# Optimization experiments

Measured on AMD Instinct MI355X. Metric: run time of the kernel, lower is better.

## Reference

```python
import jax, jax.numpy as jnp
import numpy as np

B, G, D, L, NH = 4, 30, 320, 4, 8
DK = D // NH
S = G * G
FF = 4 * D
EPS = 1e-5

FLOAT_KEYS = ['pe', 'in_emb_w', 'in_emb_b', 'wq', 'bq', 'wk', 'bk', 'wv', 'bv', 'wo', 'bo',
              'ln_a_g', 'ln_a_b', 'dist_emb', 'dir_emb', 'w_rot', 'b_rot', 'w_refl', 'b_refl',
              'w_tr', 'b_tr', 'w_sc', 'b_sc', 'tn_w1', 'tn_b1', 'tn_w2', 'tn_b2', 'tn_w3', 'tn_b3',
              'ff_w1', 'ff_b1', 'ff_w2', 'ff_b2', 'ln2_g', 'ln2_b', 'ck1', 'cb1', 'ck3', 'cb3',
              'ck5', 'cb5', 'ck7', 'cb7', 'fus_w', 'fus_b', 'op_w1', 'op_b1', 'op_w2', 'op_b2',
              'op_w3', 'op_b3']


def _make_pe():
    # Faithful vectorization of GeometricPositionalEncoding's triple loop.
    pe = np.zeros((G, G, D), dtype=np.float32)
    i = np.arange(0, D // 2, 2)                       # 0,2,...,158
    div = 10000.0 ** (i / D)
    h = np.arange(G, dtype=np.float64)
    sh = np.sin(h[:, None] / div)[:, None, :]
    ch = np.cos(h[:, None] / div)[:, None, :]
    pe[:, :, i] = sh
    pe[:, :, i + 1] = ch
    sw = np.sin(h[:, None] / div)[None, :, :]
    cw = np.cos(h[:, None] / div)[None, :, :]
    pe[:, :, i + D // 2] = sw
    pe[:, :, i + D // 2 + 1] = cw
    hh, ww = np.meshgrid(np.arange(G), np.arange(G), indexing='ij')
    c = G // 2
    pe[:, :, -4] = np.sqrt((hh - c) ** 2 + (ww - c) ** 2) / G   # overwrites last 4 dims, as in torch
    pe[:, :, -3] = hh / G
    pe[:, :, -2] = ww / G
    pe[:, :, -1] = (hh + ww) / (2 * G)
    return pe


def _make_geo_indices():
    # Precompute _compute_geometric_bias index tables (distance bin, direction octant).
    idx = np.arange(S)
    hc, wc = idx // G, idx % G
    dh = hc[None, :] - hc[:, None]                    # h2 - h1 at [i, j]
    dw = wc[None, :] - wc[:, None]
    dist = np.minimum(np.sqrt(dh ** 2 + dw ** 2).astype(np.int32), 59)
    ang = np.arctan2(dh.astype(np.float64), dw.astype(np.float64))
    dirn = ((ang + np.pi) / (2 * np.pi / 8)).astype(np.int32) % 8
    dirn[(dh == 0) & (dw == 0)] = 0
    return dist.astype(np.int32), dirn.astype(np.int32)


def _ln(x, g, b):
    m = x.mean(-1, keepdims=True)
    v = ((x - m) ** 2).mean(-1, keepdims=True)
    return (x - m) * jax.lax.rsqrt(v + EPS) * g + b


def _gelu(x):
    return jax.nn.gelu(x, approximate=False)  # torch nn.GELU default (erf)


def _forward(p, input_grid, dist_idx, dir_idx):
    x = jax.nn.one_hot(input_grid[:, 0], 10, dtype=jnp.float32)   # [B,G,G,10]
    x = x @ p['in_emb_w'] + p['in_emb_b']                          # [B,G,G,D]
    x = x + p['pe'][None]
    scale = 1.0 / np.sqrt(DK)
    for l in range(L):
        xs = x.reshape(B, S, D)
        def heads(w, b):
            return (xs @ w + b).reshape(B, S, NH, DK).transpose(0, 2, 1, 3)
        q = heads(p['wq'][l], p['bq'][l])
        k = heads(p['wk'][l], p['bk'][l])
        v = heads(p['wv'][l], p['bv'][l])
        # geometric bias via embedding gathers: [S,S,NH] -> [NH,S,S]
        bias = p['dist_emb'][l][dist_idx] + p['dir_emb'][l][dir_idx]
        scores = jnp.einsum('bhsd,bhtd->bhst', q, k) * scale + bias.transpose(2, 0, 1)[None]
        attn = jax.nn.softmax(scores, axis=-1)
        out = jnp.einsum('bhst,bhtd->bhsd', attn, v).transpose(0, 2, 1, 3).reshape(B, S, D)
        xs = _ln(out @ p['wo'][l] + p['bo'][l] + xs, p['ln_a_g'][l], p['ln_a_b'][l])
        # geometric transformation module
        g = xs.mean(1)                                              # [B,D] global mean over H,W
        tp = jnp.concatenate([
            jax.nn.softmax(g @ p['w_rot'][l] + p['b_rot'][l], axis=-1),
            jax.nn.softmax(g @ p['w_refl'][l] + p['b_refl'][l], axis=-1),
            jnp.tanh(g @ p['w_tr'][l] + p['b_tr'][l]),
            jax.nn.softmax(g @ p['w_sc'][l] + p['b_sc'][l], axis=-1)], axis=-1)   # [B,17]
        ti = jnp.concatenate([xs, jnp.broadcast_to(tp[:, None, :], (B, S, 17))], axis=-1)
        t = _gelu(ti @ p['tn_w1'][l] + p['tn_b1'][l])
        t = _gelu(t @ p['tn_w2'][l] + p['tn_b2'][l])
        t = t @ p['tn_w3'][l] + p['tn_b3'][l]
        xs = xs + 0.3 * t
        # feed-forward with post-LN residual
        f = _gelu(xs @ p['ff_w1'][l] + p['ff_b1'][l]) @ p['ff_w2'][l] + p['ff_b2'][l]
        xs = _ln(f + xs, p['ln2_g'][l], p['ln2_b'][l])
        x = xs.reshape(B, G, G, D)
    # multiscale conv fusion (NHWC, SAME padding == torch padding=k//2 for odd k)
    dn = ('NHWC', 'HWIO', 'NHWC')
    feats = [jax.nn.relu(jax.lax.conv_general_dilated(x, p['ck%d' % kk], (1, 1), 'SAME',
                                                      dimension_numbers=dn) + p['cb%d' % kk])
             for kk in (1, 3, 5, 7)]
    fused = jnp.concatenate(feats, axis=-1) @ p['fus_w'] + p['fus_b']
    h1 = _gelu(fused @ p['op_w1'] + p['op_b1'])
    h2 = _gelu(h1 @ p['op_w2'] + p['op_b2'])
    return h2 @ p['op_w3'] + p['op_b3']                            # [B,G,G,10] logits


def setup_inputs():
    key = jax.random.key(0)
    ks = iter(jax.random.split(key, 80))
    w = lambda *s: (0.02 * jax.random.normal(next(ks), s)).astype(jnp.float32)
    z = lambda *s: jnp.zeros(s, jnp.float32)
    inp = dict(
        input_grid=jax.random.randint(next(ks), (B, 1, G, G), 0, 10, dtype=jnp.int32),
        pe=jnp.asarray(_make_pe()),
        in_emb_w=w(10, D), in_emb_b=z(D),
        wq=w(L, D, D), bq=z(L, D), wk=w(L, D, D), bk=z(L, D),
        wv=w(L, D, D), bv=z(L, D), wo=w(L, D, D), bo=z(L, D),
        ln_a_g=jnp.ones((L, D), jnp.float32), ln_a_b=z(L, D),
        dist_emb=w(L, 60, NH), dir_emb=w(L, 8, NH),
        w_rot=w(L, D, 4), b_rot=z(L, 4), w_refl=w(L, D, 8), b_refl=z(L, 8),
        w_tr=w(L, D, 2), b_tr=z(L, 2), w_sc=w(L, D, 3), b_sc=z(L, 3),
        tn_w1=w(L, D + 17, 2 * D), tn_b1=z(L, 2 * D),
        tn_w2=w(L, 2 * D, D), tn_b2=z(L, D),
        tn_w3=w(L, D, D), tn_b3=z(L, D),
        ff_w1=w(L, D, FF), ff_b1=z(L, FF), ff_w2=w(L, FF, D), ff_b2=z(L, D),
        ln2_g=jnp.ones((L, D), jnp.float32), ln2_b=z(L, D),
        ck1=w(1, 1, D, D), cb1=z(D), ck3=w(3, 3, D, D), cb3=z(D),
        ck5=w(5, 5, D, D), cb5=z(D), ck7=w(7, 7, D, D), cb7=z(D),
        fus_w=w(4 * D, D), fus_b=z(D),
        op_w1=w(D, D // 2), op_b1=z(D // 2),
        op_w2=w(D // 2, D // 4), op_b2=z(D // 4),
        op_w3=w(D // 4, 10), op_b3=z(10),
    )
    di, dr = _make_geo_indices()
    inp['dist_idx'] = jnp.asarray(di)
    inp['dir_idx'] = jnp.asarray(dr)
    return inp


def reference(input_grid, dist_idx, dir_idx, pe, in_emb_w, in_emb_b, wq, bq, wk, bk, wv, bv, wo, bo,
              ln_a_g, ln_a_b, dist_emb, dir_emb, w_rot, b_rot, w_refl, b_refl, w_tr, b_tr, w_sc, b_sc,
              tn_w1, tn_b1, tn_w2, tn_b2, tn_w3, tn_b3, ff_w1, ff_b1, ff_w2, ff_b2, ln2_g, ln2_b,
              ck1, cb1, ck3, cb3, ck5, cb5, ck7, cb7, fus_w, fus_b,
              op_w1, op_b1, op_w2, op_b2, op_w3, op_b3):
    p = dict(zip(FLOAT_KEYS, (pe, in_emb_w, in_emb_b, wq, bq, wk, bk, wv, bv, wo, bo,
                              ln_a_g, ln_a_b, dist_emb, dir_emb, w_rot, b_rot, w_refl, b_refl,
                              w_tr, b_tr, w_sc, b_sc, tn_w1, tn_b1, tn_w2, tn_b2, tn_w3, tn_b3,
                              ff_w1, ff_b1, ff_w2, ff_b2, ln2_g, ln2_b, ck1, cb1, ck3, cb3,
                              ck5, cb5, ck7, cb7, fus_w, fus_b, op_w1, op_b1, op_w2, op_b2,
                              op_w3, op_b3)))
    return _forward(p, input_grid, dist_idx, dir_idx)
```

## Files before the change

### kernel.cpp

```cpp
#include <hip/hip_runtime.h>
#include <hip/hip_bf16.h>

#define BB 4
#define GG_ 30
#define DD 320
#define LL 4
#define NHH 8
#define DKK 40
#define SS 900
#define BS 3600
#define FFD 1280
#define LDK 72

typedef __attribute__((ext_vector_type(8))) short short8;
typedef __attribute__((ext_vector_type(4))) short short4v;
typedef __attribute__((ext_vector_type(4))) float f32x4;

__device__ __forceinline__ float gelu_f(float x) {
    return 0.5f * x * (1.0f + erff(x * 0.70710678118654752f));
}

__device__ __forceinline__ float bfbits2f(short b) {
    return __uint_as_float(((unsigned)(unsigned short)b) << 16);
}

__device__ __forceinline__ void convt_tile(const float* __restrict__ s,
                                           __hip_bfloat16* __restrict__ d,
                                           int K, int N, int Kpad, int kb, int nb) {
    __shared__ float t[32][33];
    const int tx = threadIdx.x, ty = threadIdx.y;
#pragma unroll
    for (int i = 0; i < 4; ++i) {
        int k = kb + ty + i * 8, n = nb + tx;
        t[ty + i * 8][tx] = (k < K && n < N) ? s[(size_t)k * N + n] : 0.f;
    }
    __syncthreads();
#pragma unroll
    for (int i = 0; i < 4; ++i) {
        int n = nb + ty + i * 8, k = kb + tx;
        if (n < N && k < Kpad) d[(size_t)n * Kpad + k] = __float2bfloat16(t[tx][ty + i * 8]);
    }
}

__global__ __launch_bounds__(256) void allconvt_kernel(
    const float* wo, const float* tnw1, const float* tnw2, const float* tnw3,
    const float* ffw1, const float* ffw2, const float* ck1, const float* ck3,
    const float* ck5, const float* ck7, const float* fusw, const float* opw1,
    __hip_bfloat16* WOT, __hip_bfloat16* TN1T, __hip_bfloat16* TN2T, __hip_bfloat16* TN3T,
    __hip_bfloat16* FF1T, __hip_bfloat16* FF2T, __hip_bfloat16* CK1T, __hip_bfloat16* CK3T,
    __hip_bfloat16* CK5T, __hip_bfloat16* CK7T, __hip_bfloat16* FUST, __hip_bfloat16* OP1T) {
    const int bid = blockIdx.x;
    const float* s; __hip_bfloat16* d;
    int K, N, Kpad, gx, per, local, sS, dS;
    if (bid < 400)        { local = bid;         s = wo;   d = WOT;  K = 320;  N = 320;  Kpad = 320;  sS = 102400; dS = 102400; gx = 10;  per = 100; }
    else if (bid < 1360)  { local = bid - 400;   s = tnw1; d = TN1T; K = 337;  N = 640;  Kpad = 384;  sS = 215680; dS = 245760; gx = 12;  per = 240; }
    else if (bid < 2160)  { local = bid - 1360;  s = tnw2; d = TN2T; K = 640;  N = 320;  Kpad = 640;  sS = 204800; dS = 204800; gx = 20;  per = 200; }
    else if (bid < 2560)  { local = bid - 2160;  s = tnw3; d = TN3T; K = 320;  N = 320;  Kpad = 320;  sS = 102400; dS = 102400; gx = 10;  per = 100; }
    else if (bid < 4160)  { local = bid - 2560;  s = ffw1; d = FF1T; K = 320;  N = 1280; Kpad = 320;  sS = 409600; dS = 409600; gx = 10;  per = 400; }
    else if (bid < 5760)  { local = bid - 4160;  s = ffw2; d = FF2T; K = 1280; N = 320;  Kpad = 1280; sS = 409600; dS = 409600; gx = 40;  per = 400; }
    else if (bid < 5860)  { local = bid - 5760;  s = ck1;  d = CK1T; K = 320;  N = 320;  Kpad = 320;  sS = 0; dS = 0; gx = 10;  per = 100; }
    else if (bid < 6760)  { local = bid - 5860;  s = ck3;  d = CK3T; K = 2880; N = 320;  Kpad = 2880; sS = 0; dS = 0; gx = 90;  per = 900; }
    else if (bid < 9260)  { local = bid - 6760;  s = ck5;  d = CK5T; K = 8000; N = 320;  Kpad = 8000; sS = 0; dS = 0; gx = 250; per = 2500; }
    else if (bid < 14160) { local = bid - 9260;  s = ck7;  d = CK7T; K = 15680; N = 320; Kpad = 15680; sS = 0; dS = 0; gx = 490; per = 4900; }
    else if (bid < 14560) { local = bid - 14160; s = fusw; d = FUST; K = 1280; N = 320;  Kpad = 1280; sS = 0; dS = 0; gx = 40;  per = 400; }
    else                  { local = bid - 14560; s = opw1; d = OP1T; K = 320;  N = 160;  Kpad = 320;  sS = 0; dS = 0; gx = 10;  per = 50; }
    const int mat = local / per, rem = local - mat * per;
    const int kb = (rem % gx) * 32, nb = (rem / gx) * 32;
    convt_tile(s + (size_t)mat * sS, d + (size_t)mat * dS, K, N, Kpad, kb, nb);
}

__global__ __launch_bounds__(256) void qkvconvt_kernel(const float* __restrict__ wq,
                                                       const float* __restrict__ wk,
                                                       const float* __restrict__ wv,
                                                       __hip_bfloat16* __restrict__ dst) {
    __shared__ float t[32][33];
    const int z = blockIdx.z, l = z / 3, wsel = z % 3;
    const float* s = (wsel == 0 ? wq : wsel == 1 ? wk : wv) + (size_t)l * 102400;
    __hip_bfloat16* d = dst + (size_t)l * 307200 + wsel * 102400;
    const int kb = blockIdx.x * 32, nb = blockIdx.y * 32;
    const int tx = threadIdx.x, ty = threadIdx.y;
#pragma unroll
    for (int i = 0; i < 4; ++i) {
        int k = kb + ty + i * 8, n = nb + tx;
        t[ty + i * 8][tx] = s[(size_t)k * 320 + n];
    }
    __syncthreads();
#pragma unroll
    for (int i = 0; i < 4; ++i) {
        int n = nb + ty + i * 8, k = kb + tx;
        d[(size_t)n * 320 + k] = __float2bfloat16(t[tx][ty + i * 8]);
    }
}

__global__ void embed_kernel(const int* __restrict__ grid, const float* __restrict__ pe,
                             const float* __restrict__ ew, const float* __restrict__ eb,
                             float* __restrict__ x, __hip_bfloat16* __restrict__ xb) {
    int idx = blockIdx.x * 256 + threadIdx.x;
    int m = idx / DD, d = idx % DD;
    int gv = grid[m];
    float v = ew[gv * DD + d] + eb[d] + pe[(m % SS) * DD + d];
    x[idx] = v;
    xb[idx] = __float2bfloat16(v);
}

__global__ __launch_bounds__(256) void mgemm_kernel(
    const __hip_bfloat16* __restrict__ A, int lda,
    const __hip_bfloat16* __restrict__ Wt, int ldw,
    const float* __restrict__ bias, const float* __restrict__ biasB, const float* __restrict__ biasC,
    const float* __restrict__ res, int ldr,
    float alpha, float* __restrict__ Cf, float* __restrict__ Cf2,
    __hip_bfloat16* __restrict__ Cb, int ldc,
    int M, int N, int K, int act) {
    __shared__ short As[128 * LDK];
    __shared__ short Bs[64 * LDK];
    const int tid = threadIdx.x;
    const int m0 = blockIdx.y * 128, n0 = blockIdx.x * 64;
    const int kb0 = blockIdx.z * K;
    float* __restrict__ CfO = (blockIdx.z == 0) ? Cf : Cf2;
    const int lane = tid & 63;
    const int w = tid >> 6, wm = w >> 1, wn = w & 1;
    const int rbase = tid >> 3, q8 = (tid & 7) * 8;
    f32x4 acc[4][2];
    const f32x4 fz = {0.f, 0.f, 0.f, 0.f};
#pragma unroll
    for (int mi = 0; mi < 4; ++mi)
#pragma unroll
        for (int ni = 0; ni < 2; ++ni) acc[mi][ni] = fz;
    const short8 zz = {0, 0, 0, 0, 0, 0, 0, 0};
    for (int k0 = 0; k0 < K; k0 += 64) {
#pragma unroll
        for (int c = 0; c < 4; ++c) {
            int r = c * 32 + rbase, m = m0 + r;
            short8 v = zz;
            if (m < M) v = *(const short8*)((const short*)A + (size_t)m * lda + kb0 + k0 + q8);
            *(short8*)(As + r * LDK + q8) = v;
        }
#pragma unroll
        for (int c = 0; c < 2; ++c) {
            int r = c * 32 + rbase, n = n0 + r;
            short8 v = zz;
            if (n < N) v = *(const short8*)((const short*)Wt + (size_t)n * ldw + kb0 + k0 + q8);
            *(short8*)(Bs + r * LDK + q8) = v;
        }
        __syncthreads();
#pragma unroll
        for (int ks = 0; ks < 64; ks += 32) {
            const int kb = ks + (lane >> 4) * 8;
            short8 af[4], bf[2];
#pragma unroll
            for (int mi = 0; mi < 4; ++mi)
                af[mi] = *(const short8*)(As + (wm * 64 + mi * 16 + (lane & 15)) * LDK + kb);
#pragma unroll
            for (int ni = 0; ni < 2; ++ni)
                bf[ni] = *(const short8*)(Bs + (wn * 32 + ni * 16 + (lane & 15)) * LDK + kb);
#pragma unroll
            for (int mi = 0; mi < 4; ++mi)
#pragma unroll
                for (int ni = 0; ni < 2; ++ni)
                    acc[mi][ni] = __builtin_amdgcn_mfma_f32_16x16x32_bf16(af[mi], bf[ni], acc[mi][ni], 0, 0, 0);
        }
        __syncthreads();
    }
    const int col0 = n0 + wn * 32 + (lane & 15);
    const int rloc = (lane >> 4) * 4;
#pragma unroll
    for (int mi = 0; mi < 4; ++mi) {
#pragma unroll
        for (int ni = 0; ni < 2; ++ni) {
            int col = col0 + ni * 16;
            if (col >= N) continue;
            float bv;
            if (biasC) bv = (col < 320) ? bias[col] : (col < 640) ? biasB[col - 320] : biasC[col - 640];
            else bv = bias ? bias[col] : 0.f;
#pragma unroll
            for (int r = 0; r < 4; ++r) {
                int row = m0 + wm * 64 + mi * 16 + rloc + r;
                if (row >= M) continue;
                float v = acc[mi][ni][r] + bv;
                if (act == 1) v = gelu_f(v);
                else if (act == 2) v = fmaxf(v, 0.f);
                v *= alpha;
                if (res) v += res[(size_t)row * ldr + col];
                if (CfO) CfO[(size_t)row * ldc + col] = v;
                if (Cb) Cb[(size_t)row * ldc + col] = __float2bfloat16(v);
            }
        }
    }
}

template <int KS>
__global__ __launch_bounds__(256) void mconv_kernel(
    const __hip_bfloat16* __restrict__ P, const __hip_bfloat16* __restrict__ Wt,
    __hip_bfloat16* __restrict__ part, int kh0step) {
    const int K = KS * KS * DD;
    const int OFF = 3 - KS / 2;
    const int nwg = 145 * gridDim.z;
    const int ib = blockIdx.x + 29 * (blockIdx.y + 5 * blockIdx.z);
    const int xcd = ib & 7, kk2 = ib >> 3;
    const int qq = nwg >> 3, rr = nwg & 7;
    const int wid = (xcd < rr) ? (xcd * (qq + 1) + kk2) : (rr * (qq + 1) + (xcd - rr) * qq + kk2);
    const int mt = wid % 29, rest = wid / 29;
    const int nt = rest % 5, zt = rest / 5;
    const int kh0 = zt * kh0step;
    const int nkh = (KS - kh0 < kh0step) ? (KS - kh0) : kh0step;
    const int wbase = kh0 * KS * DD;
    __hip_bfloat16* __restrict__ Cp = part + (size_t)zt * BS * DD;
    __shared__ short As[128 * LDK];
    __shared__ short Bs[64 * LDK];
    const int tid = threadIdx.x;
    const int m0 = mt * 128, n0 = nt * 64;
    const int lane = tid & 63;
    const int w = tid >> 6, wm = w >> 1, wn = w & 1;
    const int rbase = tid >> 3, q8 = (tid & 7) * 8;
    f32x4 acc[4][2];
    const f32x4 fz = {0.f, 0.f, 0.f, 0.f};
#pragma unroll
    for (int mi = 0; mi < 4; ++mi)
#pragma unroll
        for (int ni = 0; ni < 2; ++ni) acc[mi][ni] = fz;
    const short8 zz = {0, 0, 0, 0, 0, 0, 0, 0};
    const short* P0[4];
    bool mval[4];
#pragma unroll
    for (int c = 0; c < 4; ++c) {
        int m = m0 + c * 32 + rbase;
        mval[c] = (m < BS);
        int mm = mval[c] ? m : 0;
        int b = mm / SS, hw = mm % SS, oh = hw / GG_, ow = hw % GG_;
        P0[c] = (const short*)P + (size_t)((b * 36 + oh) * 36 + ow) * DD + q8;
    }
    const short* W0[2];
#pragma unroll
    for (int c = 0; c < 2; ++c) {
        int n = n0 + c * 32 + rbase;
        W0[c] = (const short*)Wt + (size_t)n * K + wbase + q8;
    }
    const int ntap = nkh * KS;
    for (int tap = 0; tap < ntap; ++tap) {
        const int khr = tap / KS, kw = tap - khr * KS;
        const int tapOff = (((kh0 + khr) + OFF) * 36 + (kw + OFF)) * DD;
        const int wOff = tap * DD;
        for (int ci0 = 0; ci0 < DD; ci0 += 64) {
#pragma unroll
            for (int c = 0; c < 4; ++c) {
                int r = c * 32 + rbase;
                short8 v = mval[c] ? *(const short8*)(P0[c] + tapOff + ci0) : zz;
                *(short8*)(As + r * LDK + q8) = v;
            }
#pragma unroll
            for (int c = 0; c < 2; ++c) {
                int r = c * 32 + rbase;
                short8 v = *(const short8*)(W0[c] + wOff + ci0);
                *(short8*)(Bs + r * LDK + q8) = v;
            }
            __syncthreads();
#pragma unroll
            for (int ks = 0; ks < 64; ks += 32) {
                const int kb = ks + (lane >> 4) * 8;
                short8 af[4], bf[2];
#pragma unroll
                for (int mi = 0; mi < 4; ++mi)
                    af[mi] = *(const short8*)(As + (wm * 64 + mi * 16 + (lane & 15)) * LDK + kb);
#pragma unroll
                for (int ni = 0; ni < 2; ++ni)
                    bf[ni] = *(const short8*)(Bs + (wn * 32 + ni * 16 + (lane & 15)) * LDK + kb);
#pragma unroll
                for (int mi = 0; mi < 4; ++mi)
#pragma unroll
                    for (int ni = 0; ni < 2; ++ni)
                        acc[mi][ni] = __builtin_amdgcn_mfma_f32_16x16x32_bf16(af[mi], bf[ni], acc[mi][ni], 0, 0, 0);
            }
            __syncthreads();
        }
    }
    const int col0 = n0 + wn * 32 + (lane & 15);
    const int rloc = (lane >> 4) * 4;
#pragma unroll
    for (int mi = 0; mi < 4; ++mi) {
#pragma unroll
        for (int ni = 0; ni < 2; ++ni) {
            int col = col0 + ni * 16;
#pragma unroll
            for (int r = 0; r < 4; ++r) {
                int row = m0 + wm * 64 + mi * 16 + rloc + r;
                if (row < BS) Cp[(size_t)row * DD + col] = __float2bfloat16(acc[mi][ni][r]);
            }
        }
    }
}

__global__ __launch_bounds__(256) void creduce_kernel(const __hip_bfloat16* __restrict__ part,
                                                      int nsplit, const float* __restrict__ bias,
                                                      __hip_bfloat16* __restrict__ outb, int ldc) {
    int idx = blockIdx.x * 256 + threadIdx.x;
    if (idx >= BS * DD / 8) return;
    int row = idx / (DD / 8), c8 = (idx % (DD / 8)) * 8;
    float s[8] = {};
    for (int p = 0; p < nsplit; ++p) {
        short8 v = *(const short8*)((const short*)part + (size_t)p * BS * DD + (size_t)row * DD + c8);
#pragma unroll
        for (int j = 0; j < 8; ++j) s[j] += bfbits2f(v[j]);
    }
    __hip_bfloat16* o = outb + (size_t)row * ldc + c8;
#pragma unroll
    for (int j = 0; j < 8; ++j) o[j] = __float2bfloat16(fmaxf(s[j] + bias[c8 + j], 0.f));
}

__global__ void pad_kernel(const __hip_bfloat16* __restrict__ xb, __hip_bfloat16* __restrict__ p) {
    int idx = blockIdx.x * 256 + threadIdx.x;
    if (idx >= BB * 36 * 36 * DD) return;
    int c = idx % DD, t = idx / DD;
    int wp = t % 36, t2 = t / 36, hp = t2 % 36, b = t2 / 36;
    __hip_bfloat16 v = __float2bfloat16(0.f);
    if (hp >= 3 && hp < 33 && wp >= 3 && wp < 33)
        v = xb[((b * SS + (hp - 3) * GG_ + (wp - 3))) * DD + c];
    p[idx] = v;
}

__global__ __launch_bounds__(256) void gemm_kernel(
    const float* __restrict__ A, int lda, const float* __restrict__ W,
    const float* __restrict__ bias, float* __restrict__ C, int ldc,
    int M, int N, int K, int act) {
    __shared__ float As[16][65];
    __shared__ float Ws[16][65];
    const int tid = threadIdx.x;
    const int m0 = blockIdx.y * 64, n0 = blockIdx.x * 64;
    const int tx = tid & 15, ty = tid >> 4;
    float acc[4][4] = {};
    const int kkA = tid & 15, mloc0 = tid >> 4;
    const int nloc = tid & 63, kk0 = tid >> 6;
    for (int k0 = 0; k0 < K; k0 += 16) {
        const int kA = k0 + kkA;
#pragma unroll
        for (int i = 0; i < 4; ++i) {
            int mloc = mloc0 + i * 16, m = m0 + mloc;
            As[kkA][mloc] = (m < M && kA < K) ? A[m * lda + kA] : 0.f;
        }
#pragma unroll
        for (int i = 0; i < 4; ++i) {
            int kk = kk0 + i * 4, k = k0 + kk, n = n0 + nloc;
            Ws[kk][nloc] = (k < K && n < N) ? W[k * N + n] : 0.f;
        }
        __syncthreads();
#pragma unroll
        for (int kk = 0; kk < 16; ++kk) {
            float a[4], b[4];
#pragma unroll
            for (int i = 0; i < 4; ++i) a[i] = As[kk][ty * 4 + i];
#pragma unroll
            for (int j = 0; j < 4; ++j) b[j] = Ws[kk][tx * 4 + j];
#pragma unroll
            for (int i = 0; i < 4; ++i)
#pragma unroll
                for (int j = 0; j < 4; ++j) acc[i][j] = fmaf(a[i], b[j], acc[i][j]);
        }
        __syncthreads();
    }
#pragma unroll
    for (int i = 0; i < 4; ++i) {
        int m = m0 + ty * 4 + i;
        if (m >= M) continue;
#pragma unroll
        for (int j = 0; j < 4; ++j) {
            int n = n0 + tx * 4 + j;
            if (n >= N) continue;
            float v = acc[i][j] + bias[n];
            if (act == 1) v = gelu_f(v);
            C[m * ldc + n] = v;
        }
    }
}

__global__ __launch_bounds__(256) void attprep_kernel(const float* __restrict__ de,
                                                      const float* __restrict__ dre,
                                                      const int* __restrict__ dist,
                                                      const int* __restrict__ dirn,
                                                      const __hip_bfloat16* __restrict__ QKV,
                                                      __hip_bfloat16* __restrict__ biasOut,
                                                      __hip_bfloat16* __restrict__ VT) {
    const int gid = blockIdx.x;
    const int tid = threadIdx.x;
    if (gid < 3375) {
        int idx = gid * 256 + tid;
        int sq = idx / 960, t = idx - sq * 960;
        float lut[NHH];
        if (t < SS) {
            int dv = dist[sq * SS + t], rv = dirn[sq * SS + t];
#pragma unroll
            for (int h = 0; h < NHH; ++h) lut[h] = de[dv * NHH + h] + dre[rv * NHH + h];
        } else {
#pragma unroll
            for (int h = 0; h < NHH; ++h) lut[h] = 0.f;
        }
#pragma unroll
        for (int h = 0; h < NHH; ++h)
            biasOut[((size_t)h * SS + sq) * 960 + t] = __float2bfloat16(lut[h]);
    } else {
        int vidx = (gid - 3375) * 256 + tid;
        int t0 = (vidx % 240) * 4;
        int d = (vidx / 240) % 48;
        int h = (vidx / (240 * 48)) % NHH;
        int b = vidx / (240 * 48 * NHH);
        short4v v = {0, 0, 0, 0};
        if (d < DKK) {
#pragma unroll
            for (int j = 0; j < 4; ++j) {
                int t = t0 + j;
                if (t < SS)
                    v[j] = ((const short*)QKV)[((size_t)b * SS + t) * 960 + 640 + h * DKK + d];
            }
        }
        *(short4v*)((short*)VT + (((size_t)b * NHH + h) * 48 + d) * 960 + t0) = v;
    }
}

#define LQ 72
#define LK 72
#define LV 72
#define LP 72
__global__ __launch_bounds__(512) void mattn_kernel(
    const __hip_bfloat16* __restrict__ Qg, const __hip_bfloat16* __restrict__ Kg,
    const __hip_bfloat16* __restrict__ VTg, const __hip_bfloat16* __restrict__ BIASg,
    __hip_bfloat16* __restrict__ AO) {
    const int qt = blockIdx.x, h = blockIdx.y, b = blockIdx.z;
    const int tid = threadIdx.x, lane = tid & 63, w = tid >> 6;
    const int wq = w & 3, ws = w >> 2;
    const int tid2 = tid & 255;
    const int lhi = lane >> 4, llo = lane & 15;
    __shared__ short Qs[64 * LQ];
    __shared__ short Ks[2][64 * LK];
    __shared__ short Vs[2][48 * LV];
    __shared__ short Ps[8][16 * LP];
    __shared__ float Lm[4][16];
    __shared__ float Ll[4][16];
    __shared__ float Lo[4][16][DKK];
    short* Ps_w = Ps[w];
    short* Ks_s = Ks[ws];
    short* Vs_s = Vs[ws];
    const int q0 = qt * 64;
    const short4v z4 = {0, 0, 0, 0};
    const f32x4 fz = {0.f, 0.f, 0.f, 0.f};
    const float scale = 0.15811388300841898f;

    for (int task = tid; task < 64 * 16; task += 512) {
        int r = task >> 4, d0 = (task & 15) * 4;
        int q = q0 + r;
        short4v v = z4;
        if (q < SS && d0 < DKK)
            v = *(const short4v*)((const short*)Qg + ((size_t)b * SS + q) * 960 + h * DKK + d0);
        *(short4v*)(Qs + r * LQ + d0) = v;
    }
    __syncthreads();
    short8 qa[2];
#pragma unroll
    for (int ks = 0; ks < 2; ++ks)
        qa[ks] = *(const short8*)(Qs + (wq * 16 + llo) * LQ + ks * 32 + lhi * 8);

    float mrow[4] = {-1e30f, -1e30f, -1e30f, -1e30f};
    float lrow[4] = {0.f, 0.f, 0.f, 0.f};
    f32x4 o[3] = {fz, fz, fz};
    const int qrow = q0 + wq * 16 + lhi * 4;

    for (int tt = 0; tt < 8; ++tt) {
        const int t = tt * 2 + ws;
        const int kv0 = t * 64;
        if (t < 15) {
            for (int task = tid2; task < 64 * 16; task += 256) {
                int r = task >> 4, d0 = (task & 15) * 4;
                int kv = kv0 + r;
                short4v v = z4;
                if (kv < SS && d0 < DKK)
                    v = *(const short4v*)((const short*)Kg + ((size_t)b * SS + kv) * 960 + h * DKK + d0);
                *(short4v*)(Ks_s + r * LK + d0) = v;
            }
            for (int task = tid2; task < 48 * 16; task += 256) {
                int r = task >> 4, c4 = (task & 15) * 4;
                short4v v = *(const short4v*)((const short*)VTg +
                             (((size_t)b * NHH + h) * 48 + r) * 960 + kv0 + c4);
                *(short4v*)(Vs_s + r * LV + c4) = v;
            }
        }
        __syncthreads();
        if (t < 15) {
            f32x4 s[4] = {fz, fz, fz, fz};
#pragma unroll
            for (int ks = 0; ks < 2; ++ks) {
#pragma unroll
                for (int ni = 0; ni < 4; ++ni) {
                    short8 kb = *(const short8*)(Ks_s + (ni * 16 + llo) * LK + ks * 32 + lhi * 8);
                    s[ni] = __builtin_amdgcn_mfma_f32_16x16x32_bf16(qa[ks], kb, s[ni], 0, 0, 0);
                }
            }
#pragma unroll
            for (int ni = 0; ni < 4; ++ni) {
                int col = kv0 + ni * 16 + llo;
#pragma unroll
                for (int r = 0; r < 4; ++r) {
                    int qc = qrow + r; if (qc > SS - 1) qc = SS - 1;
                    float v = s[ni][r] * scale +
                              __bfloat162float(BIASg[((size_t)h * SS + qc) * 960 + col]);
                    s[ni][r] = (col < SS) ? v : -1e30f;
                }
            }
            float rmax[4], psum[4], corr[4];
#pragma unroll
            for (int r = 0; r < 4; ++r)
                rmax[r] = fmaxf(fmaxf(s[0][r], s[1][r]), fmaxf(s[2][r], s[3][r]));
#pragma unroll
            for (int off = 1; off < 16; off <<= 1)
#pragma unroll
                for (int r = 0; r < 4; ++r)
                    rmax[r] = fmaxf(rmax[r], __shfl_xor(rmax[r], off));
#pragma unroll
            for (int r = 0; r < 4; ++r) {
                float mnew = fmaxf(mrow[r], rmax[r]);
                corr[r] = __expf(mrow[r] - mnew);
                mrow[r] = mnew;
                float ps = 0.f;
#pragma unroll
                for (int ni = 0; ni < 4; ++ni) {
                    float p = __expf(s[ni][r] - mnew);
                    s[ni][r] = p;
                    ps += p;
                }
                psum[r] = ps;
            }
#pragma unroll
            for (int off = 1; off < 16; off <<= 1)
#pragma unroll
                for (int r = 0; r < 4; ++r) psum[r] += __shfl_xor(psum[r], off);
#pragma unroll
            for (int r = 0; r < 4; ++r) lrow[r] = lrow[r] * corr[r] + psum[r];
#pragma unroll
            for (int nj = 0; nj < 3; ++nj)
#pragma unroll
                for (int r = 0; r < 4; ++r) o[nj][r] *= corr[r];
#pragma unroll
            for (int ni = 0; ni < 4; ++ni)
#pragma unroll
                for (int r = 0; r < 4; ++r)
                    ((__hip_bfloat16*)Ps_w)[(lhi * 4 + r) * LP + ni * 16 + llo] =
                        __float2bfloat16(s[ni][r]);
#pragma unroll
            for (int ks = 0; ks < 2; ++ks) {
                short8 pa = *(const short8*)(Ps_w + llo * LP + ks * 32 + lhi * 8);
#pragma unroll
                for (int nj = 0; nj < 3; ++nj) {
                    short8 vb = *(const short8*)(Vs_s + (nj * 16 + llo) * LV + ks * 32 + lhi * 8);
                    o[nj] = __builtin_amdgcn_mfma_f32_16x16x32_bf16(pa, vb, o[nj], 0, 0, 0);
                }
            }
        }
        __syncthreads();
    }
    if (ws == 1) {
#pragma unroll
        for (int r = 0; r < 4; ++r) {
            int lr = lhi * 4 + r;
            if (llo == 0) { Lm[wq][lr] = mrow[r]; Ll[wq][lr] = lrow[r]; }
#pragma unroll
            for (int nj = 0; nj < 3; ++nj) {
                int d = nj * 16 + llo;
                if (d < DKK) Lo[wq][lr][d] = o[nj][r];
            }
        }
    }
    __syncthreads();
    if (ws == 0) {
#pragma unroll
        for (int r = 0; r < 4; ++r) {
            int lr = lhi * 4 + r;
            float m1 = Lm[wq][lr], l1 = Ll[wq][lr];
            float m = fmaxf(mrow[r], m1);
            float a0 = __expf(mrow[r] - m), a1 = __expf(m1 - m);
            float linv = 1.f / (lrow[r] * a0 + l1 * a1);
            int q = qrow + r;
            if (q < SS) {
#pragma unroll
                for (int nj = 0; nj < 3; ++nj) {
                    int d = nj * 16 + llo;
                    if (d < DKK)
                        AO[((size_t)b * SS + q) * DD + h * DKK + d] =
                            __float2bfloat16((o[nj][r] * a0 + Lo[wq][lr][d] * a1) * linv);
                }
            }
        }
    }
}

__global__ __launch_bounds__(320) void ln_kernel(const float* __restrict__ a,
                                                 const float* __restrict__ a2,
                                                 const float* __restrict__ cb,
                                                 const float* __restrict__ add,
                                                 const float* __restrict__ g,
                                                 const float* __restrict__ bta,
                                                 float* __restrict__ out,
                                                 __hip_bfloat16* __restrict__ outb) {
    const int row = blockIdx.x, i = threadIdx.x;
    __shared__ float red[320];
    __shared__ float s_m, s_v;
    float v = a[row * DD + i];
    if (a2) v += a2[row * DD + i];
    if (cb) v += cb[i];
    if (add) v += add[row * DD + i];
    red[i] = v;
    __syncthreads();
    if (i < 64) red[i] += red[i + 256];
    __syncthreads();
    for (int s = 128; s > 0; s >>= 1) {
        if (i < s) red[i] += red[i + s];
        __syncthreads();
    }
    if (i == 0) s_m = red[0] * (1.0f / DD);
    __syncthreads();
    const float d = v - s_m;
    red[i] = d * d;
    __syncthreads();
    if (i < 64) red[i] += red[i + 256];
    __syncthreads();
    for (int s = 128; s > 0; s >>= 1) {
        if (i < s) red[i] += red[i + s];
        __syncthreads();
    }
    if (i == 0) s_v = red[0] * (1.0f / DD);
    __syncthreads();
    float o = d * rsqrtf(s_v + 1e-5f) * g[i] + bta[i];
    out[row * DD + i] = o;
    outb[row * DD + i] = __float2bfloat16(o);
}

__global__ __launch_bounds__(256) void mpart_kernel(const float* __restrict__ xs,
                                                    float* __restrict__ mp) {
    const int b = blockIdx.y, z = blockIdx.z;
    const int d = blockIdx.x * 64 + (threadIdx.x & 63);
    const int rg = threadIdx.x >> 6;
    float s = 0.f;
    const int t0 = z * 150;
    for (int t = t0 + rg; t < t0 + 150; t += 4) s += xs[((size_t)b * SS + t) * DD + d];
    __shared__ float red[256];
    red[threadIdx.x] = s;
    __syncthreads();
    if (threadIdx.x < 128) red[threadIdx.x] += red[threadIdx.x + 128];
    __syncthreads();
    if (threadIdx.x < 64) mp[((size_t)b * 6 + z) * DD + d] = red[threadIdx.x] + red[threadIdx.x + 64];
}

__global__ __launch_bounds__(64) void tp_kernel(const float* __restrict__ mp,
                                                const float* __restrict__ wrot, const float* __restrict__ brot,
                                                const float* __restrict__ wrefl, const float* __restrict__ brefl,
                                                const float* __restrict__ wtr, const float* __restrict__ btr,
                                                const float* __restrict__ wsc, const float* __restrict__ bsc,
                                                float* __restrict__ tp) {
    const int b = blockIdx.x, tid = threadIdx.x;
    __shared__ float gs[DD];
    __shared__ float raw[17];
    for (int j = tid; j < DD; j += 64) {
        float s6 = 0.f;
#pragma unroll
        for (int z = 0; z < 6; ++z) s6 += mp[((size_t)b * 6 + z) * DD + j];
        gs[j] = s6 * (1.0f / SS);
    }
    __syncthreads();
    if (tid < 17) {
        float s;
        if (tid < 4) {
            s = brot[tid];
            for (int d = 0; d < DD; ++d) s = fmaf(gs[d], wrot[d * 4 + tid], s);
        } else if (tid < 12) {
            int j = tid - 4;
            s = brefl[j];
            for (int d = 0; d < DD; ++d) s = fmaf(gs[d], wrefl[d * 8 + j], s);
        } else if (tid < 14) {
            int j = tid - 12;
            s = btr[j];
            for (int d = 0; d < DD; ++d) s = fmaf(gs[d], wtr[d * 2 + j], s);
        } else {
            int j = tid - 14;
            s = bsc[j];
            for (int d = 0; d < DD; ++d) s = fmaf(gs[d], wsc[d * 3 + j], s);
        }
        raw[tid] = s;
    }
    __syncthreads();
    if (tid == 0) {
        float mx = -1e30f;
        for (int j = 0; j < 4; ++j) mx = fmaxf(mx, raw[j]);
        float sm = 0.f, e[4];
        for (int j = 0; j < 4; ++j) { e[j] = expf(raw[j] - mx); sm += e[j]; }
        for (int j = 0; j < 4; ++j) tp[b * 17 + j] = e[j] / sm;
    } else if (tid == 1) {
        float mx = -1e30f;
        for (int j = 4; j < 12; ++j) mx = fmaxf(mx, raw[j]);
        float sm = 0.f, e[8];
        for (int j = 0; j < 8; ++j) { e[j] = expf(raw[4 + j] - mx); sm += e[j]; }
        for (int j = 0; j < 8; ++j) tp[b * 17 + 4 + j] = e[j] / sm;
    } else if (tid == 2) {
        tp[b * 17 + 12] = tanhf(raw[12]);
        tp[b * 17 + 13] = tanhf(raw[13]);
    } else if (tid == 3) {
        float mx = -1e30f;
        for (int j = 14; j < 17; ++j) mx = fmaxf(mx, raw[j]);
        float sm = 0.f, e[3];
        for (int j = 0; j < 3; ++j) { e[j] = expf(raw[14 + j] - mx); sm += e[j]; }
        for (int j = 0; j < 3; ++j) tp[b * 17 + 14 + j] = e[j] / sm;
    }
}

__global__ void concat_kernel(const __hip_bfloat16* __restrict__ xb, const float* __restrict__ tp,
                              __hip_bfloat16* __restrict__ ti) {
    int idx = blockIdx.x * 256 + threadIdx.x;
    if (idx >= BS * 384) return;
    int m = idx / 384, j = idx % 384;
    __hip_bfloat16 v;
    if (j < DD) v = xb[m * DD + j];
    else if (j < 337) v = __float2bfloat16(tp[(m / SS) * 17 + (j - DD)]);
    else v = __float2bfloat16(0.f);
    ti[idx] = v;
}

static inline void launch_mgemm(hipStream_t s, const __hip_bfloat16* A, int lda,
                                const __hip_bfloat16* Wt, int ldw, const float* bias,
                                const float* biasB, const float* biasC,
                                const float* res, int ldr, float alpha, float* Cf,
                                __hip_bfloat16* Cb, int ldc, int M, int N, int K, int act) {
    dim3 g((N + 63) / 64, (M + 127) / 128);
    mgemm_kernel<<<g, 256, 0, s>>>(A, lda, Wt, ldw, bias, biasB, biasC, res, ldr, alpha,
                                   Cf, nullptr, Cb, ldc, M, N, K, act);
}

extern "C" void kernel_launch(void* const* d_in, const int* in_sizes, int n_in,
                              void* d_out, int out_size, void* d_ws, size_t ws_size,
                              hipStream_t stream) {
    (void)in_sizes; (void)n_in; (void)out_size; (void)ws_size;
    const int* in_grid = (const int*)d_in[0];
    const float* pe = (const float*)d_in[1];
    const float* iew = (const float*)d_in[2];
    const float* ieb = (const float*)d_in[3];
    const float* wq = (const float*)d_in[4], *bq = (const float*)d_in[5];
    const float* wk = (const float*)d_in[6], *bk = (const float*)d_in[7];
    const float* wv = (const float*)d_in[8], *bv = (const float*)d_in[9];
    const float* wo = (const float*)d_in[10], *bo = (const float*)d_in[11];
    const float* lnag = (const float*)d_in[12], *lnab = (const float*)d_in[13];
    const float* dist_emb = (const float*)d_in[14], *dir_emb = (const float*)d_in[15];
    const float* wrot = (const float*)d_in[16], *brot = (const float*)d_in[17];
    const float* wrefl = (const float*)d_in[18], *brefl = (const float*)d_in[19];
    const float* wtr = (const float*)d_in[20], *btr = (const float*)d_in[21];
    const float* wsc = (const float*)d_in[22], *bsc = (const float*)d_in[23];
    const float* tnw1 = (const float*)d_in[24], *tnb1 = (const float*)d_in[25];
    const float* tnw2 = (const float*)d_in[26], *tnb2 = (const float*)d_in[27];
    const float* tnw3 = (const float*)d_in[28], *tnb3 = (const float*)d_in[29];
    const float* ffw1 = (const float*)d_in[30], *ffb1 = (const float*)d_in[31];
    const float* ffw2 = (const float*)d_in[32], *ffb2 = (const float*)d_in[33];
    const float* ln2g = (const float*)d_in[34], *ln2b = (const float*)d_in[35];
    const float* ck1 = (const float*)d_in[36], *cb1 = (const float*)d_in[37];
    const float* ck3 = (const float*)d_in[38], *cb3 = (const float*)d_in[39];
    const float* ck5 = (const float*)d_in[40], *cb5 = (const float*)d_in[41];
    const float* ck7 = (const float*)d_in[42], *cb7 = (const float*)d_in[43];
    const float* fusw = (const float*)d_in[44], *fusb = (const float*)d_in[45];
    const float* opw1 = (const float*)d_in[46], *opb1 = (const float*)d_in[47];
    const float* opw2 = (const float*)d_in[48], *opb2 = (const float*)d_in[49];
    const float* opw3 = (const float*)d_in[50], *opb3 = (const float*)d_in[51];
    const int* dist_idx = (const int*)d_in[52];
    const int* dir_idx = (const int*)d_in[53];
    float* out = (float*)d_out;

    char* base = (char*)d_ws;
    typedef __hip_bfloat16 bf;
    bf* WQKVT = (bf*)(base + 0);
    bf* WOT = (bf*)(base + 2457600);
    bf* TN1T = (bf*)(base + 3276800);
    bf* TN2T = (bf*)(base + 5242880);
    bf* TN3T = (bf*)(base + 6881280);
    bf* FF1T = (bf*)(base + 7700480);
    bf* FF2T = (bf*)(base + 10977280);
    bf* CK1T = (bf*)(base + 14254080);
    bf* CK3T = (bf*)(base + 14458880);
    bf* CK5T = (bf*)(base + 16302080);
    bf* CK7T = (bf*)(base + 21422080);
    bf* FUST = (bf*)(base + 31457280);
    bf* OP1T = (bf*)(base + 32276480);
    float* XS = (float*)(base + 32378880);
    bf* XSbf = (bf*)(base + 36986880);
    bf* QKVbf = (bf*)(base + 39290880);
    bf* VT = (bf*)(base + 46202880);
    float* P1f = (float*)(base + 39290880);
    float* R2 = (float*)(base + 53114880);
    float* TP = (float*)(base + 57728000);
    bf* CPART = (bf*)(base + 39290880);
    char* BIG = base + 57728512;
    bf* AObf = (bf*)(BIG + 0);
    float* MPart = (float*)(BIG + 0);
    bf* BIAS = (bf*)(BIG + 2764800);
    bf* TIbf = (bf*)(BIG + 0);
    bf* T1bf = (bf*)(BIG + 2764800);
    bf* T2bf = (bf*)(BIG + 7372800);
    bf* F1bf = (bf*)(BIG + 0);
    bf* PADbf = (bf*)(BIG + 0);
    bf* FEATSbf = (bf*)(BIG + 3317760);
    float* H1 = (float*)(BIG + 0);
    float* H2 = (float*)(BIG + 2304000);
    bf* R2bf = XSbf;

    dim3 cb(32, 8);
    qkvconvt_kernel<<<dim3(10, 10, 12), cb, 0, stream>>>(wq, wk, wv, WQKVT);
    allconvt_kernel<<<14610, cb, 0, stream>>>(wo, tnw1, tnw2, tnw3, ffw1, ffw2,
                                              ck1, ck3, ck5, ck7, fusw, opw1,
                                              WOT, TN1T, TN2T, TN3T, FF1T, FF2T,
                                              CK1T, CK3T, CK5T, CK7T, FUST, OP1T);

    embed_kernel<<<4500, 256, 0, stream>>>(in_grid, pe, iew, ieb, XS, XSbf);

    for (int l = 0; l < LL; ++l) {
        const int wO = l * DD * DD, bO = l * DD;
        launch_mgemm(stream, XSbf, DD, WQKVT + l * 307200, 320, bq + bO, bk + bO, bv + bO,
                     nullptr, 0, 1.f, nullptr, QKVbf, 960, BS, 960, 320, 0);
        attprep_kernel<<<4815, 256, 0, stream>>>(dist_emb + l * 60 * NHH, dir_emb + l * 8 * NHH,
                                                 dist_idx, dir_idx, QKVbf, BIAS, VT);
        mattn_kernel<<<dim3(15, NHH, BB), 512, 0, stream>>>(QKVbf, QKVbf + 320, VT, BIAS, AObf);
        launch_mgemm(stream, AObf, DD, WOT + wO, DD, bo + bO, nullptr, nullptr, XS, DD, 1.f,
                     R2, nullptr, DD, BS, DD, DD, 0);
        ln_kernel<<<BS, 320, 0, stream>>>(R2, nullptr, nullptr, nullptr, lnag + bO, lnab + bO, XS, XSbf);
        mpart_kernel<<<dim3(5, BB, 6), 256, 0, stream>>>(XS, MPart);
        tp_kernel<<<BB, 64, 0, stream>>>(MPart, wrot + l * 1280, brot + l * 4,
                                         wrefl + l * 2560, brefl + l * 8,
                                         wtr + l * 640, btr + l * 2,
                                         wsc + l * 960, bsc + l * 3, TP);
        concat_kernel<<<(BS * 384 + 255) / 256, 256, 0, stream>>>(XSbf, TP, TIbf);
        launch_mgemm(stream, TIbf, 384, TN1T + l * 245760, 384, tnb1 + l * 640, nullptr, nullptr,
                     nullptr, 0, 1.f, nullptr, T1bf, 640, BS, 640, 384, 1);
        launch_mgemm(stream, T1bf, 640, TN2T + l * 204800, 640, tnb2 + bO, nullptr, nullptr,
                     nullptr, 0, 1.f, nullptr, T2bf, DD, BS, DD, 640, 1);
        launch_mgemm(stream, T2bf, DD, TN3T + wO, DD, tnb3 + bO, nullptr, nullptr, XS, DD, 0.3f,
                     XS, XSbf, DD, BS, DD, DD, 0);
        launch_mgemm(stream, XSbf, DD, FF1T + l * 409600, DD, ffb1 + l * FFD, nullptr, nullptr,
                     nullptr, 0, 1.f, nullptr, F1bf, FFD, BS, FFD, DD, 1);
        {
            dim3 g(5, 29, 2);
            mgemm_kernel<<<g, 256, 0, stream>>>(F1bf, FFD, FF2T + l * 409600, FFD,
                                                nullptr, nullptr, nullptr, nullptr, 0, 1.f,
                                                R2, P1f, nullptr, DD, BS, DD, 640, 0);
        }
        ln_kernel<<<BS, 320, 0, stream>>>(R2, P1f, ffb2 + bO, XS, ln2g + bO, ln2b + bO, XS, XSbf);
    }

    pad_kernel<<<(BB * 36 * 36 * DD + 255) / 256, 256, 0, stream>>>(XSbf, PADbf);
    launch_mgemm(stream, XSbf, DD, CK1T, DD, cb1, nullptr, nullptr, nullptr, 0, 1.f,
                 nullptr, FEATSbf + 0, 1280, BS, DD, DD, 2);
    const int RED = (BS * DD / 8 + 255) / 256;
    mconv_kernel<3><<<dim3(29, 5, 3), 256, 0, stream>>>(PADbf, CK3T, CPART, 1);
    creduce_kernel<<<RED, 256, 0, stream>>>(CPART, 3, cb3, FEATSbf + 320, 1280);
    mconv_kernel<5><<<dim3(29, 5, 5), 256, 0, stream>>>(PADbf, CK5T, CPART, 1);
    creduce_kernel<<<RED, 256, 0, stream>>>(CPART, 5, cb5, FEATSbf + 640, 1280);
    mconv_kernel<7><<<dim3(29, 5, 7), 256, 0, stream>>>(PADbf, CK7T, CPART, 1);
    creduce_kernel<<<RED, 256, 0, stream>>>(CPART, 7, cb7, FEATSbf + 960, 1280);
    launch_mgemm(stream, FEATSbf, 1280, FUST, 1280, fusb, nullptr, nullptr, nullptr, 0, 1.f,
                 nullptr, R2bf, DD, BS, DD, 1280, 0);
    launch_mgemm(stream, R2bf, DD, OP1T, DD, opb1, nullptr, nullptr, nullptr, 0, 1.f,
                 H1, nullptr, 160, BS, 160, DD, 1);
    gemm_kernel<<<dim3(2, 57), 256, 0, stream>>>(H1, 160, opw2, opb2, H2, 80, BS, 80, 160, 1);
    gemm_kernel<<<dim3(1, 57), 256, 0, stream>>>(H2, 80, opw3, opb3, out, 10, BS, 10, 80, 0);
}
```

Before: 1.552 ms.

## Fuse the 3x3, 5x5 and 7x7 conv GEMMs and their reductions into single launches

Replaces three templated multi-scale conv kernels and three reduction kernels with one combined conv kernel over 870 workgroups and one combined reduce kernel. The K split is coarsened to chunks of up to three kernel rows, giving 6 partial slices instead of 15, which cuts partial-sum writes and reads. The goal is fewer launches, better GPU fill, and less partial traffic. In exchange, KS becomes a runtime value, so inner loops may lose unrolling, and the segments have uneven work per workgroup.

```diff
diff --git a/kernel.cpp b/kernel.cpp
--- a/kernel.cpp
+++ b/kernel.cpp
@@ -188,23 +188,26 @@
     }
 }
 
-template <int KS>
-__global__ __launch_bounds__(256) void mconv_kernel(
-    const __hip_bfloat16* __restrict__ P, const __hip_bfloat16* __restrict__ Wt,
-    __hip_bfloat16* __restrict__ part, int kh0step) {
-    const int K = KS * KS * DD;
-    const int OFF = 3 - KS / 2;
-    const int nwg = 145 * gridDim.z;
-    const int ib = blockIdx.x + 29 * (blockIdx.y + 5 * blockIdx.z);
+__global__ __launch_bounds__(256) void mconvall_kernel(
+    const __hip_bfloat16* __restrict__ P, const __hip_bfloat16* __restrict__ W3,
+    const __hip_bfloat16* __restrict__ W5, const __hip_bfloat16* __restrict__ W7,
+    __hip_bfloat16* __restrict__ part) {
+    const int nwg = 870;
+    const int ib = blockIdx.x;
     const int xcd = ib & 7, kk2 = ib >> 3;
     const int qq = nwg >> 3, rr = nwg & 7;
     const int wid = (xcd < rr) ? (xcd * (qq + 1) + kk2) : (rr * (qq + 1) + (xcd - rr) * qq + kk2);
-    const int mt = wid % 29, rest = wid / 29;
-    const int nt = rest % 5, zt = rest / 5;
-    const int kh0 = zt * kh0step;
-    const int nkh = (KS - kh0 < kh0step) ? (KS - kh0) : kh0step;
+    const int seg = wid / 145, local = wid - seg * 145;
+    int KS, kh0, nkh, slice;
+    const __hip_bfloat16* Wt;
+    if (seg == 0)      { KS = 3; Wt = W3; kh0 = 0; nkh = 3; slice = 0; }
+    else if (seg <= 2) { KS = 5; Wt = W5; int z = seg - 1; kh0 = 3 * z; nkh = (z == 0) ? 3 : 2; slice = 1 + z; }
+    else               { KS = 7; Wt = W7; int z = seg - 3; kh0 = 3 * z; nkh = (z < 2) ? 3 : 1; slice = 3 + z; }
+    const int K = KS * KS * DD;
+    const int OFF = 3 - KS / 2;
+    const int mt = local % 29, nt = local / 29;
     const int wbase = kh0 * KS * DD;
-    __hip_bfloat16* __restrict__ Cp = part + (size_t)zt * BS * DD;
+    __hip_bfloat16* __restrict__ Cp = part + (size_t)slice * BS * DD;
     __shared__ short As[128 * LDK];
     __shared__ short Bs[64 * LDK];
     const int tid = threadIdx.x;
@@ -289,19 +292,30 @@
     }
 }
 
-__global__ __launch_bounds__(256) void creduce_kernel(const __hip_bfloat16* __restrict__ part,
-                                                      int nsplit, const float* __restrict__ bias,
-                                                      __hip_bfloat16* __restrict__ outb, int ldc) {
+__global__ __launch_bounds__(256) void creduceall_kernel(const __hip_bfloat16* __restrict__ part,
+                                                         const float* __restrict__ cb3,
+                                                         const float* __restrict__ cb5,
+                                                         const float* __restrict__ cb7,
+                                                         __hip_bfloat16* __restrict__ feats) {
+    const int PER = BS * DD / 8;
     int idx = blockIdx.x * 256 + threadIdx.x;
-    if (idx >= BS * DD / 8) return;
-    int row = idx / (DD / 8), c8 = (idx % (DD / 8)) * 8;
+    int which = idx / PER;
+    if (which >= 3) return;
+    int sub = idx - which * PER;
+    int row = sub / (DD / 8), c8 = (sub % (DD / 8)) * 8;
+    const __hip_bfloat16* basep;
+    const float* bias;
+    int nsplit, colOff;
+    if (which == 0)      { basep = part;                          nsplit = 1; bias = cb3; colOff = 320; }
+    else if (which == 1) { basep = part + (size_t)1 * BS * DD;    nsplit = 2; bias = cb5; colOff = 640; }
+    else                 { basep = part + (size_t)3 * BS * DD;    nsplit = 3; bias = cb7; colOff = 960; }
     float s[8] = {};
     for (int p = 0; p < nsplit; ++p) {
-        short8 v = *(const short8*)((const short*)part + (size_t)p * BS * DD + (size_t)row * DD + c8);
+        short8 v = *(const short8*)((const short*)basep + (size_t)p * BS * DD + (size_t)row * DD + c8);
 #pragma unroll
         for (int j = 0; j < 8; ++j) s[j] += bfbits2f(v[j]);
     }
-    __hip_bfloat16* o = outb + (size_t)row * ldc + c8;
+    __hip_bfloat16* o = feats + (size_t)row * 1280 + colOff + c8;
 #pragma unroll
     for (int j = 0; j < 8; ++j) o[j] = __float2bfloat16(fmaxf(s[j] + bias[c8 + j], 0.f));
 }
@@ -846,13 +860,8 @@
     pad_kernel<<<(BB * 36 * 36 * DD + 255) / 256, 256, 0, stream>>>(XSbf, PADbf);
     launch_mgemm(stream, XSbf, DD, CK1T, DD, cb1, nullptr, nullptr, nullptr, 0, 1.f,
                  nullptr, FEATSbf + 0, 1280, BS, DD, DD, 2);
-    const int RED = (BS * DD / 8 + 255) / 256;
-    mconv_kernel<3><<<dim3(29, 5, 3), 256, 0, stream>>>(PADbf, CK3T, CPART, 1);
-    creduce_kernel<<<RED, 256, 0, stream>>>(CPART, 3, cb3, FEATSbf + 320, 1280);
-    mconv_kernel<5><<<dim3(29, 5, 5), 256, 0, stream>>>(PADbf, CK5T, CPART, 1);
-    creduce_kernel<<<RED, 256, 0, stream>>>(CPART, 5, cb5, FEATSbf + 640, 1280);
-    mconv_kernel<7><<<dim3(29, 5, 7), 256, 0, stream>>>(PADbf, CK7T, CPART, 1);
-    creduce_kernel<<<RED, 256, 0, stream>>>(CPART, 7, cb7, FEATSbf + 960, 1280);
+    mconvall_kernel<<<870, 256, 0, stream>>>(PADbf, CK3T, CK5T, CK7T, CPART);
+    creduceall_kernel<<<(3 * BS * DD / 8 + 255) / 256, 256, 0, stream>>>(CPART, cb3, cb5, cb7, FEATSbf);
     launch_mgemm(stream, FEATSbf, 1280, FUST, 1280, fusb, nullptr, nullptr, nullptr, 0, 1.f,
                  nullptr, R2bf, DD, BS, DD, 1280, 0);
     launch_mgemm(stream, R2bf, DD, OP1T, DD, opb1, nullptr, nullptr, nullptr, 0, 1.f,
```

Result: no change. 1.582 ms (+2.0%).
